# Kernel tuning notes

Measured on AMD Instinct MI355X. Metric: run time of the kernel, lower is better.

The kernel has to match this reference:

```python
import jax, jax.numpy as jnp
import numpy as np

CELL = 4  # 2 ** cell_2_pow, cell_2_pow = 2
EPS = 1e-5


def conv2d(x, w, b):
    # 3x3 conv, padding 1, NCHW / OIHW
    y = jax.lax.conv_general_dilated(
        x, w, window_strides=(1, 1), padding=((1, 1), (1, 1)),
        dimension_numbers=('NCHW', 'OIHW', 'NCHW'))
    return y + b[None, :, None, None]


def setup_inputs() -> dict:
    key = jax.random.key(0)
    ks = jax.random.split(key, 4)
    B, Cc, H, W = 8, 128, 512, 512
    nh, nw = H // CELL, W // CELL  # ctrl spatial must be padded_img / cell_sz
    return dict(
        image_pipe=jax.random.normal(ks[0], (B, 6, H, W), jnp.float32),
        ctrl_pipe=jax.random.normal(ks[1], (B, Cc, nh, nw), jnp.float32),
        w1=jax.random.normal(ks[2], (50, Cc, 3, 3), jnp.float32) * 0.03,
        b1=jnp.zeros((50,), jnp.float32),
        gamma=jnp.ones((50,), jnp.float32),
        beta=jnp.zeros((50,), jnp.float32),
        mean=jnp.zeros((50,), jnp.float32),
        var=jnp.ones((50,), jnp.float32),
        w2=jax.random.normal(ks[3], (18, 50, 3, 3), jnp.float32) * 0.05,
        b2=jnp.zeros((18,), jnp.float32),
    )


def reference(image_pipe, ctrl_pipe, w1, b1, gamma, beta, mean, var, w2, b2):
    cs = CELL
    B, C6, H, W = image_pipe.shape
    # conv_condense: Conv(Cc->50) -> ReLU -> BatchNorm2d(50, inference) -> Conv(50->18)
    h = jax.nn.relu(conv2d(ctrl_pipe, w1, b1))
    scale = gamma * jax.lax.rsqrt(var + EPS)
    h = (h - mean[None, :, None, None]) * scale[None, :, None, None] + beta[None, :, None, None]
    cond = conv2d(h, w2, b2)  # [B, 18, nh, nw]
    nh, nw = cond.shape[-2], cond.shape[-1]

    padH = (-H) % cs
    padW = (-W) % cs
    rH, rW = H + padH, W + padW
    # F.pad(img, (cell, padW+cell, cell, padH+cell)): left/right then top/bottom
    img = jnp.pad(image_pipe, ((0, 0), (0, 0), (cs, padH + cs), (cs, padW + cs)))

    # 9 cell-strided shifted views; torch loop order: i over width (outer), j over height (inner)
    stack = jnp.stack(
        [img[:, :, j * cs:j * cs + rH, i * cs:i * cs + rW]
         for i in range(3) for j in range(3)], axis=-1)  # [B, 6, rH, rW, 9]
    stack = stack.reshape(B, 2, 3, rH, rW, 9)  # 2 groups of 3 channels

    # per-pixel dynamic 9-tap weights, constant within each cs x cs cell
    wts = cond.reshape(B, 2, 9, nh, nw)
    wts = jnp.repeat(jnp.repeat(wts, cs, axis=3), cs, axis=4)  # [B, 2, 9, rH, rW]

    out = jnp.einsum('bgchwk,bgkhw->bgchw', stack, wts)  # weighted neighborhood sum
    out = out.reshape(B, 6, rH, rW)[:, :, :H, :W]
    return out
```

## Files before the change

### kernel.cpp

```cpp
#include <hip/hip_runtime.h>

typedef __attribute__((ext_vector_type(8))) short short8;
typedef __attribute__((ext_vector_type(4))) float floatx4;

__device__ __forceinline__ unsigned short f2bf(float f) {
    union { float f; unsigned int u; } v; v.f = f;
    unsigned int r = (v.u + 0x7fffu + ((v.u >> 16) & 1u)) >> 16;
    return (unsigned short)r;
}

__device__ __forceinline__ float4 shfl4(float4 v, int srcLane) {
    float4 r;
    r.x = __shfl(v.x, srcLane, 64);
    r.y = __shfl(v.y, srcLane, 64);
    r.z = __shfl(v.z, srcLane, 64);
    r.w = __shfl(v.w, srcLane, 64);
    return r;
}

__global__ __launch_bounds__(256) void transpose_kernel(
    const float* __restrict__ ctrl, unsigned short* __restrict__ ctrlT)
{
    __shared__ unsigned short tile[64 * 66];
    const int t = threadIdx.x;
    const int x0 = blockIdx.x * 64, ci0 = blockIdx.y * 64;
    const int b = blockIdx.z >> 7, y = blockIdx.z & 127;
#pragma unroll
    for (int it = 0; it < 4; it++) {
        int ci_l = it * 16 + (t >> 4);
        int x_l = (t & 15) * 4;
        const float4 v = *(const float4*)&ctrl[(((size_t)b * 128 + ci0 + ci_l) * 128 + y) * 128 + x0 + x_l];
        tile[(x_l + 0) * 66 + ci_l] = f2bf(v.x);
        tile[(x_l + 1) * 66 + ci_l] = f2bf(v.y);
        tile[(x_l + 2) * 66 + ci_l] = f2bf(v.z);
        tile[(x_l + 3) * 66 + ci_l] = f2bf(v.w);
    }
    __syncthreads();
#pragma unroll
    for (int it = 0; it < 2; it++) {
        int x_l = it * 32 + (t >> 3);
        int ci_l = (t & 7) * 8;
        const unsigned int* p = (const unsigned int*)&tile[x_l * 66 + ci_l];
        uint4 u = make_uint4(p[0], p[1], p[2], p[3]);
        *(uint4*)&ctrlT[(((size_t)b * 128 + y) * 128 + x0 + x_l) * 128 + ci0 + ci_l] = u;
    }
}

__global__ __launch_bounds__(256) void prep_w_kernel(
    const float* __restrict__ w1, const float* __restrict__ w2,
    unsigned short* __restrict__ w1p, unsigned short* __restrict__ w2p)
{
    int i = blockIdx.x * 256 + threadIdx.x;
    if (i < 4 * 9 * 64 * 32) {
        int ci = i & 31; int t2 = i >> 5; int co = t2 & 63; int t3 = t2 >> 6;
        int tap = t3 % 9; int c4 = t3 / 9;
        float v = 0.f;
        if (co < 50) v = w1[((size_t)co * 128 + c4 * 32 + ci) * 9 + tap];
        w1p[i] = f2bf(v);
    } else {
        int j = i - 4 * 9 * 64 * 32;
        int ci = j & 31; int t2 = j >> 5; int co = t2 & 31; int t3 = t2 >> 5;
        int tap = t3 % 9; int c4 = t3 / 9;
        int cig = c4 * 32 + ci;
        float v = 0.f;
        if (co < 18 && cig < 50) v = w2[((size_t)co * 50 + cig) * 9 + tap];
        w2p[j] = f2bf(v);
    }
}

__global__ __launch_bounds__(256) void conv1_mfma(
    const unsigned short* __restrict__ xT, const unsigned short* __restrict__ w1p,
    const float* __restrict__ b1, const float* __restrict__ gamma,
    const float* __restrict__ beta, const float* __restrict__ mean,
    const float* __restrict__ var, unsigned short* __restrict__ h)
{
    __shared__ unsigned short in_s[324 * 40];
    __shared__ unsigned short w_s[9 * 64 * 40];
    const int tid = threadIdx.x;
    const int x0 = blockIdx.x * 16, y0 = blockIdx.y * 16, b = blockIdx.z;
    const int wid = tid >> 6, lane = tid & 63;
    const int ln = lane & 15, q = lane >> 4;

    floatx4 acc[4][4];
#pragma unroll
    for (int mt = 0; mt < 4; mt++)
#pragma unroll
        for (int nt = 0; nt < 4; nt++) acc[mt][nt] = (floatx4)(0.f);

    for (int c4 = 0; c4 < 4; c4++) {
        for (int i = tid; i < 1296; i += 256) {
            int p = i >> 2, g = i & 3;
            int gy = y0 + p / 18 - 1, gx = x0 + p % 18 - 1;
            uint4 v = make_uint4(0, 0, 0, 0);
            if (gy >= 0 && gy < 128 && gx >= 0 && gx < 128)
                v = *(const uint4*)&xT[(((size_t)b * 128 + gy) * 128 + gx) * 128 + c4 * 32 + g * 8];
            *(uint4*)&in_s[p * 40 + g * 8] = v;
        }
#pragma unroll
        for (int it = 0; it < 9; it++) {
            int f = it * 256 + tid;
            int g = f & 3, co = (f >> 2) & 63, tap = f >> 8;
            uint4 v = *(const uint4*)&w1p[(((size_t)c4 * 9 + tap) * 64 + co) * 32 + g * 8];
            *(uint4*)&w_s[(tap * 64 + co) * 40 + g * 8] = v;
        }
        __syncthreads();

#pragma unroll
        for (int tap = 0; tap < 9; tap++) {
            const int dy = tap / 3, dx = tap % 3;
            short8 a[4];
#pragma unroll
            for (int mt = 0; mt < 4; mt++)
                a[mt] = *(const short8*)&in_s[((wid * 4 + mt + dy) * 18 + ln + dx) * 40 + q * 8];
#pragma unroll
            for (int nt = 0; nt < 4; nt++) {
                short8 bf = *(const short8*)&w_s[(tap * 64 + nt * 16 + ln) * 40 + q * 8];
#pragma unroll
                for (int mt = 0; mt < 4; mt++)
                    acc[mt][nt] = __builtin_amdgcn_mfma_f32_16x16x32_bf16(a[mt], bf, acc[mt][nt], 0, 0, 0);
            }
        }
        __syncthreads();
    }

#pragma unroll
    for (int nt = 0; nt < 4; nt++) {
        int co = nt * 16 + ln;
        bool real = co < 50;
        float sc = 0.f, mn = 0.f, bt = 0.f, bs = 0.f;
        if (real) {
            sc = gamma[co] * rsqrtf(var[co] + 1e-5f);
            mn = mean[co]; bt = beta[co]; bs = b1[co];
        }
#pragma unroll
        for (int mt = 0; mt < 4; mt++) {
            int gy = y0 + wid * 4 + mt;
#pragma unroll
            for (int r = 0; r < 4; r++) {
                int px = q * 4 + r;
                float v = 0.f;
                if (real) {
                    float tv = fmaxf(acc[mt][nt][r] + bs, 0.f);
                    v = (tv - mn) * sc + bt;
                }
                h[(((size_t)b * 128 + gy) * 128 + x0 + px) * 64 + co] = f2bf(v);
            }
        }
    }
}

__global__ __launch_bounds__(256) void conv2_mfma(
    const unsigned short* __restrict__ hT, const unsigned short* __restrict__ w2p,
    const float* __restrict__ b2, float* __restrict__ cond)
{
    __shared__ unsigned short in_s[324 * 40];
    __shared__ unsigned short w_s[9 * 32 * 40];
    const int tid = threadIdx.x;
    const int x0 = blockIdx.x * 16, y0 = blockIdx.y * 16, b = blockIdx.z;
    const int wid = tid >> 6, lane = tid & 63;
    const int ln = lane & 15, q = lane >> 4;

    floatx4 acc[4][2];
#pragma unroll
    for (int mt = 0; mt < 4; mt++)
#pragma unroll
        for (int nt = 0; nt < 2; nt++) acc[mt][nt] = (floatx4)(0.f);

    for (int c4 = 0; c4 < 2; c4++) {
        for (int i = tid; i < 1296; i += 256) {
            int p = i >> 2, g = i & 3;
            int gy = y0 + p / 18 - 1, gx = x0 + p % 18 - 1;
            uint4 v = make_uint4(0, 0, 0, 0);
            if (gy >= 0 && gy < 128 && gx >= 0 && gx < 128)
                v = *(const uint4*)&hT[(((size_t)b * 128 + gy) * 128 + gx) * 64 + c4 * 32 + g * 8];
            *(uint4*)&in_s[p * 40 + g * 8] = v;
        }
#pragma unroll
        for (int it = 0; it < 5; it++) {
            int f = it * 256 + tid;
            if (f < 1152) {
                int g = f & 3, co = (f >> 2) & 31, tap = f >> 7;
                uint4 v = *(const uint4*)&w2p[(((size_t)c4 * 9 + tap) * 32 + co) * 32 + g * 8];
                *(uint4*)&w_s[(tap * 32 + co) * 40 + g * 8] = v;
            }
        }
        __syncthreads();

#pragma unroll
        for (int tap = 0; tap < 9; tap++) {
            const int dy = tap / 3, dx = tap % 3;
            short8 a[4];
#pragma unroll
            for (int mt = 0; mt < 4; mt++)
                a[mt] = *(const short8*)&in_s[((wid * 4 + mt + dy) * 18 + ln + dx) * 40 + q * 8];
#pragma unroll
            for (int nt = 0; nt < 2; nt++) {
                short8 bf = *(const short8*)&w_s[(tap * 32 + nt * 16 + ln) * 40 + q * 8];
#pragma unroll
                for (int mt = 0; mt < 4; mt++)
                    acc[mt][nt] = __builtin_amdgcn_mfma_f32_16x16x32_bf16(a[mt], bf, acc[mt][nt], 0, 0, 0);
            }
        }
        __syncthreads();
    }

#pragma unroll
    for (int nt = 0; nt < 2; nt++) {
        int co = nt * 16 + ln;
        if (co < 18) {
            float bs = b2[co];
            int gch = co / 9, k = co % 9;
            int iw = k / 3, jy = k % 3;
            int pos = gch * 12 + jy * 4 + iw;
#pragma unroll
            for (int mt = 0; mt < 4; mt++) {
                int gy = y0 + wid * 4 + mt;
#pragma unroll
                for (int r = 0; r < 4; r++) {
                    int px = q * 4 + r;
                    cond[(((size_t)b * 128 + gy) * 128 + x0 + px) * 24 + pos] = acc[mt][nt][r] + bs;
                }
            }
        }
    }
}

__global__ __launch_bounds__(256) void apply_kernel(
    const float* __restrict__ img, const float* __restrict__ cond,
    float* __restrict__ out)
{
    const int tid = threadIdx.x;
    const int xl = tid & 63, s = tid >> 6;
    const int x4 = blockIdx.x * 64 + xl;
    const int o = blockIdx.y * 4 + s;
    const int b = blockIdx.z >> 1, g = blockIdx.z & 1;
    const int cy = o >> 2;
    const int laneL = (xl + 63) & 63, laneR = (xl + 1) & 63;
    const bool isL = (xl == 0), isR = (xl == 63);
    const bool eok = (isL && x4 > 0) || (isR && x4 < 127);
    const int xo = x4 * 4;
    const int xe = isL ? xo - 4 : xo + 4;

    const float* cw = &cond[(((size_t)b * 128 + cy) * 128 + x4) * 24 + g * 12];
    float4 w[3];
    w[0] = *(const float4*)&cw[0];
    w[1] = *(const float4*)&cw[4];
    w[2] = *(const float4*)&cw[8];

    float4 v[3][3], e[3][3];
#pragma unroll
    for (int jy = 0; jy < 3; jy++) {
        const int r = o - 4 + 4 * jy;
        const bool rok = (r >= 0) && (r < 512);
#pragma unroll
        for (int cc = 0; cc < 3; cc++) {
            v[jy][cc] = make_float4(0.f, 0.f, 0.f, 0.f);
            e[jy][cc] = make_float4(0.f, 0.f, 0.f, 0.f);
            if (rok) {
                const float* rp = &img[((((size_t)b * 6 + g * 3 + cc) * 512) + r) * 512];
                v[jy][cc] = *(const float4*)&rp[xo];
                if (eok) e[jy][cc] = *(const float4*)&rp[xe];
            }
        }
    }

    float4 acc[3];
#pragma unroll
    for (int cc = 0; cc < 3; cc++) acc[cc] = make_float4(0.f, 0.f, 0.f, 0.f);

#pragma unroll
    for (int jy = 0; jy < 3; jy++) {
        const float4 wj = w[jy];
#pragma unroll
        for (int cc = 0; cc < 3; cc++) {
            float4 vc = v[jy][cc];
            float4 vL = shfl4(vc, laneL);
            float4 vR = shfl4(vc, laneR);
            if (isL) vL = e[jy][cc];
            if (isR) vR = e[jy][cc];
            acc[cc].x += vL.x * wj.x + vc.x * wj.y + vR.x * wj.z;
            acc[cc].y += vL.y * wj.x + vc.y * wj.y + vR.y * wj.z;
            acc[cc].z += vL.z * wj.x + vc.z * wj.y + vR.z * wj.z;
            acc[cc].w += vL.w * wj.x + vc.w * wj.y + vR.w * wj.z;
        }
    }

#pragma unroll
    for (int cc = 0; cc < 3; cc++)
        *(float4*)&out[((((size_t)b * 6 + g * 3 + cc) * 512) + o) * 512 + xo] = acc[cc];
}

extern "C" void kernel_launch(void* const* d_in, const int* in_sizes, int n_in,
                              void* d_out, int out_size, void* d_ws, size_t ws_size,
                              hipStream_t stream)
{
    const float* img   = (const float*)d_in[0];
    const float* ctrl  = (const float*)d_in[1];
    const float* w1    = (const float*)d_in[2];
    const float* b1    = (const float*)d_in[3];
    const float* gamma = (const float*)d_in[4];
    const float* beta  = (const float*)d_in[5];
    const float* mean  = (const float*)d_in[6];
    const float* var   = (const float*)d_in[7];
    const float* w2    = (const float*)d_in[8];
    const float* b2    = (const float*)d_in[9];
    float* out = (float*)d_out;

    char* ws = (char*)d_ws;
    unsigned short* ctrlT = (unsigned short*)ws;
    float*          cond  = (float*)ws;
    unsigned short* hbuf  = (unsigned short*)(ws + 33554432);
    unsigned short* w1p   = (unsigned short*)(ws + 50331648);
    unsigned short* w2p   = (unsigned short*)(ws + 50479104);

    transpose_kernel<<<dim3(2, 2, 1024), 256, 0, stream>>>(ctrl, ctrlT);
    prep_w_kernel<<<360, 256, 0, stream>>>(w1, w2, w1p, w2p);
    conv1_mfma<<<dim3(8, 8, 8), 256, 0, stream>>>(ctrlT, w1p, b1, gamma, beta, mean, var, hbuf);
    conv2_mfma<<<dim3(8, 8, 8), 256, 0, stream>>>(hbuf, w2p, b2, cond);
    apply_kernel<<<dim3(2, 128, 16), 256, 0, stream>>>(img, cond, out);
}
```

Measured before the change: 226.7 us.

## Register-prefetch conv tiles, relayout cond, remap apply blocks, drop shuffles

Conv1 and conv2 now prefetch the next channel chunk of input (and weights) into registers while the MFMAs run on the current chunk. Conv2 also loads both weight chunks up front. The cond buffer is laid out per group so each apply thread reads 12 contiguous floats. The apply kernel replaces cross-lane shuffles with direct left and right neighbour float4 loads, and remaps a 1D grid so consecutive hardware blocks spread across chiplets. This trades higher register pressure and redundant cached global loads for less LDS stall time and shuffle work.

```diff
diff --git a/kernel.cpp b/kernel.cpp
--- a/kernel.cpp
+++ b/kernel.cpp
@@ -7,15 +7,6 @@
     union { float f; unsigned int u; } v; v.f = f;
     unsigned int r = (v.u + 0x7fffu + ((v.u >> 16) & 1u)) >> 16;
     return (unsigned short)r;
-}
-
-__device__ __forceinline__ float4 shfl4(float4 v, int srcLane) {
-    float4 r;
-    r.x = __shfl(v.x, srcLane, 64);
-    r.y = __shfl(v.y, srcLane, 64);
-    r.z = __shfl(v.z, srcLane, 64);
-    r.w = __shfl(v.w, srcLane, 64);
-    return r;
 }
 
 __global__ __launch_bounds__(256) void transpose_kernel(
@@ -87,24 +78,53 @@
 #pragma unroll
         for (int nt = 0; nt < 4; nt++) acc[mt][nt] = (floatx4)(0.f);
 
-    for (int c4 = 0; c4 < 4; c4++) {
-        for (int i = tid; i < 1296; i += 256) {
-            int p = i >> 2, g = i & 3;
-            int gy = y0 + p / 18 - 1, gx = x0 + p % 18 - 1;
-            uint4 v = make_uint4(0, 0, 0, 0);
-            if (gy >= 0 && gy < 128 && gx >= 0 && gx < 128)
-                v = *(const uint4*)&xT[(((size_t)b * 128 + gy) * 128 + gx) * 128 + c4 * 32 + g * 8];
-            *(uint4*)&in_s[p * 40 + g * 8] = v;
-        }
+    uint4 in_r[6], w_r[9];
+    auto load_in = [&](int c4) {
+#pragma unroll
+        for (int k = 0; k < 6; k++) {
+            int i = tid + k * 256;
+            if (i < 1296) {
+                int p = i >> 2, g = i & 3;
+                int gy = y0 + p / 18 - 1, gx = x0 + p % 18 - 1;
+                in_r[k] = make_uint4(0, 0, 0, 0);
+                if (gy >= 0 && gy < 128 && gx >= 0 && gx < 128)
+                    in_r[k] = *(const uint4*)&xT[(((size_t)b * 128 + gy) * 128 + gx) * 128 + c4 * 32 + g * 8];
+            }
+        }
+    };
+    auto load_w = [&](int c4) {
 #pragma unroll
         for (int it = 0; it < 9; it++) {
             int f = it * 256 + tid;
             int g = f & 3, co = (f >> 2) & 63, tap = f >> 8;
-            uint4 v = *(const uint4*)&w1p[(((size_t)c4 * 9 + tap) * 64 + co) * 32 + g * 8];
-            *(uint4*)&w_s[(tap * 64 + co) * 40 + g * 8] = v;
-        }
-        __syncthreads();
-
+            w_r[it] = *(const uint4*)&w1p[(((size_t)c4 * 9 + tap) * 64 + co) * 32 + g * 8];
+        }
+    };
+    auto write_in = [&]() {
+#pragma unroll
+        for (int k = 0; k < 6; k++) {
+            int i = tid + k * 256;
+            if (i < 1296) {
+                int p = i >> 2, g = i & 3;
+                *(uint4*)&in_s[p * 40 + g * 8] = in_r[k];
+            }
+        }
+    };
+    auto write_w = [&]() {
+#pragma unroll
+        for (int it = 0; it < 9; it++) {
+            int f = it * 256 + tid;
+            int g = f & 3, co = (f >> 2) & 63, tap = f >> 8;
+            *(uint4*)&w_s[(tap * 64 + co) * 40 + g * 8] = w_r[it];
+        }
+    };
+
+    load_in(0); load_w(0);
+    write_in(); write_w();
+    __syncthreads();
+
+    for (int c4 = 0; c4 < 4; c4++) {
+        if (c4 < 3) { load_in(c4 + 1); load_w(c4 + 1); }
 #pragma unroll
         for (int tap = 0; tap < 9; tap++) {
             const int dy = tap / 3, dx = tap % 3;
@@ -121,6 +141,7 @@
             }
         }
         __syncthreads();
+        if (c4 < 3) { write_in(); write_w(); __syncthreads(); }
     }
 
 #pragma unroll
@@ -154,7 +175,7 @@
     const float* __restrict__ b2, float* __restrict__ cond)
 {
     __shared__ unsigned short in_s[324 * 40];
-    __shared__ unsigned short w_s[9 * 32 * 40];
+    __shared__ unsigned short w_s[2][9 * 32 * 40];
     const int tid = threadIdx.x;
     const int x0 = blockIdx.x * 16, y0 = blockIdx.y * 16, b = blockIdx.z;
     const int wid = tid >> 6, lane = tid & 63;
@@ -166,26 +187,46 @@
 #pragma unroll
         for (int nt = 0; nt < 2; nt++) acc[mt][nt] = (floatx4)(0.f);
 
+    uint4 in_r[6];
+    auto load_in = [&](int c4) {
+#pragma unroll
+        for (int k = 0; k < 6; k++) {
+            int i = tid + k * 256;
+            if (i < 1296) {
+                int p = i >> 2, g = i & 3;
+                int gy = y0 + p / 18 - 1, gx = x0 + p % 18 - 1;
+                in_r[k] = make_uint4(0, 0, 0, 0);
+                if (gy >= 0 && gy < 128 && gx >= 0 && gx < 128)
+                    in_r[k] = *(const uint4*)&hT[(((size_t)b * 128 + gy) * 128 + gx) * 64 + c4 * 32 + g * 8];
+            }
+        }
+    };
+    auto write_in = [&]() {
+#pragma unroll
+        for (int k = 0; k < 6; k++) {
+            int i = tid + k * 256;
+            if (i < 1296) {
+                int p = i >> 2, g = i & 3;
+                *(uint4*)&in_s[p * 40 + g * 8] = in_r[k];
+            }
+        }
+    };
+
+    load_in(0);
+#pragma unroll
+    for (int it = 0; it < 9; it++) {
+        int f = it * 256 + tid;
+        int c4w = f >= 1152 ? 1 : 0;
+        int f2 = f - c4w * 1152;
+        int g = f2 & 3, co = (f2 >> 2) & 31, tap = f2 >> 7;
+        uint4 v = *(const uint4*)&w2p[(((size_t)c4w * 9 + tap) * 32 + co) * 32 + g * 8];
+        *(uint4*)&w_s[c4w][(tap * 32 + co) * 40 + g * 8] = v;
+    }
+    write_in();
+    __syncthreads();
+
     for (int c4 = 0; c4 < 2; c4++) {
-        for (int i = tid; i < 1296; i += 256) {
-            int p = i >> 2, g = i & 3;
-            int gy = y0 + p / 18 - 1, gx = x0 + p % 18 - 1;
-            uint4 v = make_uint4(0, 0, 0, 0);
-            if (gy >= 0 && gy < 128 && gx >= 0 && gx < 128)
-                v = *(const uint4*)&hT[(((size_t)b * 128 + gy) * 128 + gx) * 64 + c4 * 32 + g * 8];
-            *(uint4*)&in_s[p * 40 + g * 8] = v;
-        }
-#pragma unroll
-        for (int it = 0; it < 5; it++) {
-            int f = it * 256 + tid;
-            if (f < 1152) {
-                int g = f & 3, co = (f >> 2) & 31, tap = f >> 7;
-                uint4 v = *(const uint4*)&w2p[(((size_t)c4 * 9 + tap) * 32 + co) * 32 + g * 8];
-                *(uint4*)&w_s[(tap * 32 + co) * 40 + g * 8] = v;
-            }
-        }
-        __syncthreads();
-
+        if (c4 < 1) load_in(1);
 #pragma unroll
         for (int tap = 0; tap < 9; tap++) {
             const int dy = tap / 3, dx = tap % 3;
@@ -195,13 +236,17 @@
                 a[mt] = *(const short8*)&in_s[((wid * 4 + mt + dy) * 18 + ln + dx) * 40 + q * 8];
 #pragma unroll
             for (int nt = 0; nt < 2; nt++) {
-                short8 bf = *(const short8*)&w_s[(tap * 32 + nt * 16 + ln) * 40 + q * 8];
+                short8 bf = *(const short8*)&w_s[c4][(tap * 32 + nt * 16 + ln) * 40 + q * 8];
 #pragma unroll
                 for (int mt = 0; mt < 4; mt++)
                     acc[mt][nt] = __builtin_amdgcn_mfma_f32_16x16x32_bf16(a[mt], bf, acc[mt][nt], 0, 0, 0);
             }
         }
-        __syncthreads();
+        if (c4 < 1) {
+            __syncthreads();
+            write_in();
+            __syncthreads();
+        }
     }
 
 #pragma unroll
@@ -211,14 +256,14 @@
             float bs = b2[co];
             int gch = co / 9, k = co % 9;
             int iw = k / 3, jy = k % 3;
-            int pos = gch * 12 + jy * 4 + iw;
 #pragma unroll
             for (int mt = 0; mt < 4; mt++) {
                 int gy = y0 + wid * 4 + mt;
 #pragma unroll
                 for (int r = 0; r < 4; r++) {
                     int px = q * 4 + r;
-                    cond[(((size_t)b * 128 + gy) * 128 + x0 + px) * 24 + pos] = acc[mt][nt][r] + bs;
+                    cond[((((size_t)b * 2 + gch) * 128 + gy) * 128 + (x0 + px)) * 12 + jy * 4 + iw]
+                        = acc[mt][nt][r] + bs;
                 }
             }
         }
@@ -229,37 +274,38 @@
     const float* __restrict__ img, const float* __restrict__ cond,
     float* __restrict__ out)
 {
+    const int hwid = blockIdx.x;
+    const int lid = (hwid & 7) * 512 + (hwid >> 3);
+    const int bx = lid & 1, by = (lid >> 1) & 127, bz = lid >> 8;
+
     const int tid = threadIdx.x;
     const int xl = tid & 63, s = tid >> 6;
-    const int x4 = blockIdx.x * 64 + xl;
-    const int o = blockIdx.y * 4 + s;
-    const int b = blockIdx.z >> 1, g = blockIdx.z & 1;
-    const int cy = o >> 2;
-    const int laneL = (xl + 63) & 63, laneR = (xl + 1) & 63;
-    const bool isL = (xl == 0), isR = (xl == 63);
-    const bool eok = (isL && x4 > 0) || (isR && x4 < 127);
+    const int x4 = bx * 64 + xl;
+    const int o = by * 4 + s;
+    const int b = bz >> 1, g = bz & 1;
     const int xo = x4 * 4;
-    const int xe = isL ? xo - 4 : xo + 4;
-
-    const float* cw = &cond[(((size_t)b * 128 + cy) * 128 + x4) * 24 + g * 12];
-    float4 w[3];
-    w[0] = *(const float4*)&cw[0];
-    w[1] = *(const float4*)&cw[4];
-    w[2] = *(const float4*)&cw[8];
-
-    float4 v[3][3], e[3][3];
+
+    const float* cw = &cond[((((size_t)b * 2 + g) * 128 + by) * 128 + x4) * 12];
+    float4 w0 = *(const float4*)&cw[0];
+    float4 w1 = *(const float4*)&cw[4];
+    float4 w2 = *(const float4*)&cw[8];
+
+    float4 C[3][3], L[3][3], R[3][3];
+    const bool lok = (x4 > 0), rok_x = (x4 < 127);
 #pragma unroll
     for (int jy = 0; jy < 3; jy++) {
         const int r = o - 4 + 4 * jy;
-        const bool rok = (r >= 0) && (r < 512);
+        const bool rk = (r >= 0) && (r < 512);
 #pragma unroll
         for (int cc = 0; cc < 3; cc++) {
-            v[jy][cc] = make_float4(0.f, 0.f, 0.f, 0.f);
-            e[jy][cc] = make_float4(0.f, 0.f, 0.f, 0.f);
-            if (rok) {
+            C[jy][cc] = make_float4(0.f, 0.f, 0.f, 0.f);
+            L[jy][cc] = make_float4(0.f, 0.f, 0.f, 0.f);
+            R[jy][cc] = make_float4(0.f, 0.f, 0.f, 0.f);
+            if (rk) {
                 const float* rp = &img[((((size_t)b * 6 + g * 3 + cc) * 512) + r) * 512];
-                v[jy][cc] = *(const float4*)&rp[xo];
-                if (eok) e[jy][cc] = *(const float4*)&rp[xe];
+                C[jy][cc] = *(const float4*)&rp[xo];
+                if (lok)   L[jy][cc] = *(const float4*)&rp[xo - 4];
+                if (rok_x) R[jy][cc] = *(const float4*)&rp[xo + 4];
             }
         }
     }
@@ -270,18 +316,14 @@
 
 #pragma unroll
     for (int jy = 0; jy < 3; jy++) {
-        const float4 wj = w[jy];
+        const float4 wj = (jy == 0) ? w0 : (jy == 1) ? w1 : w2;
 #pragma unroll
         for (int cc = 0; cc < 3; cc++) {
-            float4 vc = v[jy][cc];
-            float4 vL = shfl4(vc, laneL);
-            float4 vR = shfl4(vc, laneR);
-            if (isL) vL = e[jy][cc];
-            if (isR) vR = e[jy][cc];
-            acc[cc].x += vL.x * wj.x + vc.x * wj.y + vR.x * wj.z;
-            acc[cc].y += vL.y * wj.x + vc.y * wj.y + vR.y * wj.z;
-            acc[cc].z += vL.z * wj.x + vc.z * wj.y + vR.z * wj.z;
-            acc[cc].w += vL.w * wj.x + vc.w * wj.y + vR.w * wj.z;
+            const float4 l = L[jy][cc], c = C[jy][cc], r = R[jy][cc];
+            acc[cc].x += l.x * wj.x + c.x * wj.y + r.x * wj.z;
+            acc[cc].y += l.y * wj.x + c.y * wj.y + r.y * wj.z;
+            acc[cc].z += l.z * wj.x + c.z * wj.y + r.z * wj.z;
+            acc[cc].w += l.w * wj.x + c.w * wj.y + r.w * wj.z;
         }
     }
 
@@ -317,5 +359,5 @@
     prep_w_kernel<<<360, 256, 0, stream>>>(w1, w2, w1p, w2p);
     conv1_mfma<<<dim3(8, 8, 8), 256, 0, stream>>>(ctrlT, w1p, b1, gamma, beta, mean, var, hbuf);
     conv2_mfma<<<dim3(8, 8, 8), 256, 0, stream>>>(hbuf, w2p, b2, cond);
-    apply_kernel<<<dim3(2, 128, 16), 256, 0, stream>>>(img, cond, out);
-}
+    apply_kernel<<<4096, 256, 0, stream>>>(img, cond, out);
+}
```

New measurement: 243.6 us. +7.4%, slower.
